# Kernel optimization log

Measured on AMD Instinct MI355X. Metric: run time of the kernel, lower is better.

## Reference

```python
import jax, jax.numpy as jnp
import numpy as np
from jax import lax

B, C, D, H, W = 2, 1, 128, 128, 128
CONSCIOUSNESS_WEIGHT = 0.1


def _field(depth, height, width, dtype):
    # sin(2*pi*(d+h+w)/(D+H+W)) broadcast over batch/channel
    d = jnp.arange(depth, dtype=dtype)[:, None, None]
    h = jnp.arange(height, dtype=dtype)[None, :, None]
    w = jnp.arange(width, dtype=dtype)[None, None, :]
    phase = 2.0 * jnp.pi * (d + h + w) / (depth + height + width)
    return jnp.sin(phase)  # [D,H,W]


def _conv3d(x, w, b):
    y = lax.conv_general_dilated(
        x, w, window_strides=(1, 1, 1), padding='SAME',
        dimension_numbers=('NCDHW', 'OIDHW', 'NCDHW'))
    return y + b[None, :, None, None, None]


def setup_inputs() -> dict:
    key = jax.random.key(0)
    ks = jax.random.split(key, 4)
    fan1 = 1 * 27
    fan2 = 8 * 27
    fan3 = 16 * 27
    return {
        'cube_data': jax.random.normal(ks[0], (B, C, D, H, W), dtype=jnp.float32),
        'w1': jax.random.normal(ks[1], (8, 1, 3, 3, 3), dtype=jnp.float32) / np.sqrt(fan1),
        'b1': jnp.zeros((8,), dtype=jnp.float32),
        'w2': jax.random.normal(ks[2], (16, 8, 3, 3, 3), dtype=jnp.float32) / np.sqrt(fan2),
        'b2': jnp.zeros((16,), dtype=jnp.float32),
        'w3': jax.random.normal(ks[3], (1, 16, 3, 3, 3), dtype=jnp.float32) / np.sqrt(fan3),
        'b3': jnp.zeros((1,), dtype=jnp.float32),
    }


def reference(cube_data, w1, b1, w2, b2, w3, b3):
    _, _, d, h, w = cube_data.shape
    field = _field(d, h, w, cube_data.dtype)[None, None]  # [1,1,D,H,W]
    integrated = cube_data * (1.0 + CONSCIOUSNESS_WEIGHT * field)
    x = jax.nn.relu(_conv3d(integrated, w1, b1))
    x = jax.nn.relu(_conv3d(x, w2, b2))
    x = jnp.tanh(_conv3d(x, w3, b3))
    return x
```

## Files before the change

### kernel.cpp

```cpp
#include <hip/hip_runtime.h>
#include <hip/hip_fp16.h>

#define VOX (128 * 128 * 128)
#define P 130
#define PP (P * P)
#define PVOX (P * P * P)
#define LROW 130
#define PLANE (6 * LROW)

typedef unsigned short u16;
typedef _Float16 f16x2 __attribute__((ext_vector_type(2)));
typedef _Float16 f16x8 __attribute__((ext_vector_type(8)));
typedef __attribute__((ext_vector_type(4))) float f32x4;

__device__ __forceinline__ u16 f2h(float f) {
    return __builtin_bit_cast(unsigned short, (_Float16)f);
}
__device__ __forceinline__ unsigned pkh_relu(float a, float b) {
    float ra = a > 0.f ? a : 0.f, rb = b > 0.f ? b : 0.f;
    return (unsigned)f2h(ra) | ((unsigned)f2h(rb) << 16);
}
__device__ __forceinline__ f16x2 h2(unsigned u) { return __builtin_bit_cast(f16x2, u); }

__device__ __forceinline__ float dot2(unsigned a, unsigned b, float c) {
#if __has_builtin(__builtin_amdgcn_fdot2)
    return __builtin_amdgcn_fdot2(h2(a), h2(b), c, false);
#else
    f16x2 av = h2(a), bv = h2(b);
    c = fmaf((float)av.x, (float)bv.x, c);
    return fmaf((float)av.y, (float)bv.y, c);
#endif
}

__device__ __forceinline__ float fast_tanh(float x) {
    float e = __expf(2.0f * x);
    return 1.0f - 2.0f * __builtin_amdgcn_rcpf(1.0f + e);
}

__device__ __forceinline__ void gload_lds16(const u16* g, u16* l) {
    __builtin_amdgcn_global_load_lds(
        (const __attribute__((address_space(1))) unsigned int*)g,
        (__attribute__((address_space(3))) unsigned int*)l,
        16, 0, 0);
}

__global__ __launch_bounds__(256) void integrate_kernel(
    const float* __restrict__ in, u16* __restrict__ x0,
    const float* __restrict__ w1, const float* __restrict__ w2,
    const float* __restrict__ w3, u16* __restrict__ w2frag,
    unsigned* __restrict__ w3p, float* __restrict__ w1c,
    u16* __restrict__ x1, u16* __restrict__ x2) {
    int i = blockIdx.x * 256 + threadIdx.x;
    if (i < 3584) {
        int j = i & 7, l = (i >> 3) & 63, s = i >> 9;
        int tap = s * 4 + (l >> 4), oc = l & 15;
        float v = (tap < 27) ? w2[(oc * 8 + j) * 27 + tap] : 0.0f;
        w2frag[i] = f2h(v);
    }
    if (i < 216) {
        int tap = i >> 3, j = i & 7;
        w3p[i] = (unsigned)f2h(w3[(2 * j) * 27 + tap]) |
                 ((unsigned)f2h(w3[(2 * j + 1) * 27 + tap]) << 16);
        int c = i & 7;
        w1c[i] = w1[c * 27 + tap];
    }
    if (i >= PVOX) return;
    int d = i / PP;
    int r = i - d * PP;
    int h = r / P;
    int w = r - h * P;
    const bool interior = (d >= 1 && d <= 128 && h >= 1 && h <= 128 && w >= 1 && w <= 128);
    float v = 0.0f;
    if (interior) {
        int s = (d - 1) + (h - 1) + (w - 1);
        float fld = 1.0f + 0.1f * __sinf(6.283185307179586f * (float)s / 384.0f);
        v = in[(size_t)(d - 1) * 16384 + (h - 1) * 128 + (w - 1)] * fld;
    } else {
        uint4 z = {0u, 0u, 0u, 0u};
        *(uint4*)(x1 + (size_t)i * 8) = z;
        *(uint4*)(x2 + (size_t)i * 16) = z;
        *(uint4*)(x2 + (size_t)i * 16 + 8) = z;
    }
    x0[i] = f2h(v);
}

__global__ __launch_bounds__(256) void integrate_light_kernel(
    const float* __restrict__ in, u16* __restrict__ x0) {
    const int i = blockIdx.x * 256 + threadIdx.x;
    const int d = i >> 14, h = (i >> 7) & 127, w = i & 127;
    const int s = d + h + w;
    const float fld = 1.0f + 0.1f * __sinf((float)s * 0.016362461737446838f);
    x0[(size_t)(d + 1) * PP + (h + 1) * P + (w + 1)] = f2h(in[i] * fld);
}

__global__ __launch_bounds__(256) void conv1_kernel(
    const u16* __restrict__ x0, const float* __restrict__ w1c,
    const float* __restrict__ b1, u16* __restrict__ x1) {
    const int t = blockIdx.x * 256 + threadIdx.x;
    const int w0 = (t & 63) * 2;
    const int h0 = ((t >> 6) & 31) * 4;
    const int d = t >> 11;

    float acc[4][2][8];
#pragma unroll
    for (int c = 0; c < 8; ++c) {
        const float b = b1[c];
#pragma unroll
        for (int i = 0; i < 4; ++i) { acc[i][0][c] = b; acc[i][1][c] = b; }
    }

#pragma unroll
    for (int dz = 0; dz < 3; ++dz) {
        const u16* zb = x0 + (size_t)(d + dz) * PP + (size_t)h0 * P + w0;
        const float* wz = w1c + dz * 9 * 8;
#pragma unroll
        for (int r = 0; r < 6; ++r) {
            const u16* rp = zb + r * P;
            const unsigned u0 = *(const unsigned*)rp;
            const unsigned u1 = *(const unsigned*)(rp + 2);
            float vv[4];
            vv[0] = (float)h2(u0).x; vv[1] = (float)h2(u0).y;
            vv[2] = (float)h2(u1).x; vv[3] = (float)h2(u1).y;
#pragma unroll
            for (int dy = 0; dy < 3; ++dy) {
                const int i = r - dy;
                if (i < 0 || i > 3) continue;
#pragma unroll
                for (int dx = 0; dx < 3; ++dx) {
                    const float a0 = vv[dx];
                    const float a1 = vv[dx + 1];
                    const float* wp = wz + (dy * 3 + dx) * 8;
#pragma unroll
                    for (int c = 0; c < 8; ++c) {
                        const float wt = wp[c];
                        acc[i][0][c] = fmaf(wt, a0, acc[i][0][c]);
                        acc[i][1][c] = fmaf(wt, a1, acc[i][1][c]);
                    }
                }
            }
        }
    }
    const size_t e0 = ((size_t)(d + 1) * P + (h0 + 1)) * P + (w0 + 1);
#pragma unroll
    for (int i = 0; i < 4; ++i) {
        uint4 oA, oB;
        oA.x = pkh_relu(acc[i][0][0], acc[i][0][1]);
        oA.y = pkh_relu(acc[i][0][2], acc[i][0][3]);
        oA.z = pkh_relu(acc[i][0][4], acc[i][0][5]);
        oA.w = pkh_relu(acc[i][0][6], acc[i][0][7]);
        oB.x = pkh_relu(acc[i][1][0], acc[i][1][1]);
        oB.y = pkh_relu(acc[i][1][2], acc[i][1][3]);
        oB.z = pkh_relu(acc[i][1][4], acc[i][1][5]);
        oB.w = pkh_relu(acc[i][1][6], acc[i][1][7]);
        *(uint4*)(x1 + (e0 + (size_t)i * P) * 8) = oA;
        *(uint4*)(x1 + (e0 + (size_t)i * P + 1) * 8) = oB;
    }
}

__global__ __launch_bounds__(256) void conv2_mfma_kernel(
    const u16* __restrict__ x1, const u16* __restrict__ w2frag,
    const float* __restrict__ b2, u16* __restrict__ x2) {
    __shared__ u16 sm[4 * PLANE * 8];

    const int tid = threadIdx.x;
    const int lane = tid & 63;
    const int wv = tid >> 6;
    const int q = lane >> 4;
    const int mi = lane & 15;
    const int D0 = (blockIdx.x >> 5) * 8;
    const int h0 = (blockIdx.x & 31) * 4;

    f16x8 wf[7];
#pragma unroll
    for (int s = 0; s < 7; ++s)
        wf[s] = *(const f16x8*)(w2frag + (size_t)(s * 64 + lane) * 8);

#pragma unroll
    for (int p = 0; p < 3; ++p) {
        const int pd = D0 + p;
        const int slot = pd & 3;
        const u16* gb = x1 + ((size_t)(pd * P + h0) * P) * 8;
        u16* lb = sm + (size_t)slot * PLANE * 8;
#pragma unroll
        for (int k = 0; k < 3; ++k) {
            const int u0 = wv * 64 + k * 256;
            gload_lds16(gb + (size_t)(u0 + lane) * 8, lb + (size_t)u0 * 8);
        }
        if (wv == 0 && lane < PLANE - 768)
            gload_lds16(gb + (size_t)(768 + lane) * 8, lb + (size_t)768 * 8);
    }
    __syncthreads();

    const float4 bv = *(const float4*)(b2 + q * 4);

#pragma unroll 1
    for (int i = 0; i < 8; ++i) {
        const int dout = D0 + i;

        if (i < 7) {
            const int pd = dout + 3;
            const int slot = pd & 3;
            const u16* gb = x1 + ((size_t)(pd * P + h0) * P) * 8;
            u16* lb = sm + (size_t)slot * PLANE * 8;
#pragma unroll
            for (int k = 0; k < 3; ++k) {
                const int u0 = wv * 64 + k * 256;
                gload_lds16(gb + (size_t)(u0 + lane) * 8, lb + (size_t)u0 * 8);
            }
            if (wv == 0 && lane < PLANE - 768)
                gload_lds16(gb + (size_t)(768 + lane) * 8, lb + (size_t)768 * 8);
        }

        f32x4 acc[8];
#pragma unroll
        for (int t = 0; t < 8; ++t) acc[t] = (f32x4){0.f, 0.f, 0.f, 0.f};

#pragma unroll
        for (int s = 0; s < 7; ++s) {
            int tap = s * 4 + q;
            if (tap > 26) tap = 26;
            const int dz = tap / 9;
            const int rem = tap - dz * 9;
            const int dy = rem / 3;
            const int dx = rem - dy * 3;
            const int slot = (dout + dz) & 3;
            const u16* bp = sm + ((size_t)(slot * 6 + wv + dy) * LROW + (mi + dx)) * 8;
#pragma unroll
            for (int t = 0; t < 8; ++t) {
                f16x8 act = *(const f16x8*)(bp + t * 128);
                acc[t] = __builtin_amdgcn_mfma_f32_16x16x32_f16(wf[s], act, acc[t], 0, 0, 0);
            }
        }

        const size_t obase = ((size_t)(dout + 1) * P + (h0 + wv + 1)) * P + 1;
#pragma unroll
        for (int t = 0; t < 8; ++t) {
            uint2 o;
            o.x = pkh_relu(acc[t][0] + bv.x, acc[t][1] + bv.y);
            o.y = pkh_relu(acc[t][2] + bv.z, acc[t][3] + bv.w);
            *(uint2*)(x2 + (obase + 16 * t + mi) * 16 + q * 4) = o;
        }

        if (i < 7) __syncthreads();
    }
}

__global__ __launch_bounds__(256) void conv3_kernel(
    const u16* __restrict__ x2, const unsigned* __restrict__ w3p,
    const float* __restrict__ b3, float* __restrict__ out) {
    const int t = blockIdx.x * 256 + threadIdx.x;
    const int w = t & 127;
    const int h0 = ((t >> 7) & 31) * 4;
    const int d0 = (t >> 12) * 2;

    float accA[2][4], accB[2][4];
#pragma unroll
    for (int dd = 0; dd < 2; ++dd)
#pragma unroll
        for (int i = 0; i < 4; ++i) { accA[dd][i] = 0.f; accB[dd][i] = 0.f; }

#pragma unroll 1
    for (int z = 0; z < 4; ++z) {
        const u16* zb = x2 + ((size_t)((d0 + z) * P + h0) * P + w) * 16;
#pragma unroll
        for (int r = 0; r < 6; ++r) {
            const u16* rp = zb + (size_t)r * (P * 16);
            const uint4 c0l = *(const uint4*)(rp);
            const uint4 c0h = *(const uint4*)(rp + 8);
            const uint4 c1l = *(const uint4*)(rp + 16);
            const uint4 c1h = *(const uint4*)(rp + 24);
            const uint4 c2l = *(const uint4*)(rp + 32);
            const uint4 c2h = *(const uint4*)(rp + 40);
#pragma unroll
            for (int dd = 0; dd < 2; ++dd) {
                const int dz = z - dd;
                if (dz < 0 || dz > 2) continue;
                const unsigned* wz = w3p + dz * 9 * 8;
#pragma unroll
                for (int dy = 0; dy < 3; ++dy) {
                    const int i = r - dy;
                    if (i < 0 || i > 3) continue;
                    const unsigned* wp = wz + dy * 3 * 8;
                    float a = accA[dd][i], b = accB[dd][i];
                    a = dot2(c0l.x, wp[0], a);  b = dot2(c0l.y, wp[1], b);
                    a = dot2(c0l.z, wp[2], a);  b = dot2(c0l.w, wp[3], b);
                    a = dot2(c0h.x, wp[4], a);  b = dot2(c0h.y, wp[5], b);
                    a = dot2(c0h.z, wp[6], a);  b = dot2(c0h.w, wp[7], b);
                    a = dot2(c1l.x, wp[8], a);  b = dot2(c1l.y, wp[9], b);
                    a = dot2(c1l.z, wp[10], a); b = dot2(c1l.w, wp[11], b);
                    a = dot2(c1h.x, wp[12], a); b = dot2(c1h.y, wp[13], b);
                    a = dot2(c1h.z, wp[14], a); b = dot2(c1h.w, wp[15], b);
                    a = dot2(c2l.x, wp[16], a); b = dot2(c2l.y, wp[17], b);
                    a = dot2(c2l.z, wp[18], a); b = dot2(c2l.w, wp[19], b);
                    a = dot2(c2h.x, wp[20], a); b = dot2(c2h.y, wp[21], b);
                    a = dot2(c2h.z, wp[22], a); b = dot2(c2h.w, wp[23], b);
                    accA[dd][i] = a; accB[dd][i] = b;
                }
            }
        }
    }
    const float bias = b3[0];
#pragma unroll
    for (int dd = 0; dd < 2; ++dd) {
        const size_t obase = (size_t)((d0 + dd) * 128 + h0) * 128 + w;
#pragma unroll
        for (int i = 0; i < 4; ++i)
            out[obase + (size_t)i * 128] = fast_tanh(accA[dd][i] + accB[dd][i] + bias);
    }
}

extern "C" void kernel_launch(void* const* d_in, const int* in_sizes, int n_in,
                              void* d_out, int out_size, void* d_ws, size_t ws_size,
                              hipStream_t stream) {
    const float* cube = (const float*)d_in[0];
    const float* w1 = (const float*)d_in[1];
    const float* b1 = (const float*)d_in[2];
    const float* w2 = (const float*)d_in[3];
    const float* b2 = (const float*)d_in[4];
    const float* w3 = (const float*)d_in[5];
    const float* b3 = (const float*)d_in[6];
    float* out = (float*)d_out;

    char* ws = (char*)d_ws;
    u16* w2frag = (u16*)ws;
    unsigned* w3p = (unsigned*)(ws + 7168);
    float* w1c = (float*)(ws + 8032);
    u16* x0 = (u16*)(ws + 16384);
    u16* x1 = (u16*)(ws + 16384 + (size_t)PVOX * sizeof(u16));
    u16* x2 = (u16*)(ws + 16384 + (size_t)PVOX * sizeof(u16) + (size_t)PVOX * 8 * sizeof(u16));

    for (int b = 0; b < 2; ++b) {
        if (b == 0) {
            integrate_kernel<<<dim3((PVOX + 255) / 256), dim3(256), 0, stream>>>(
                cube, x0, w1, w2, w3, w2frag, w3p, w1c, x1, x2);
        } else {
            integrate_light_kernel<<<dim3(VOX / 256), dim3(256), 0, stream>>>(
                cube + (size_t)VOX, x0);
        }
        conv1_kernel<<<dim3(VOX / 8 / 256), dim3(256), 0, stream>>>(x0, w1c, b1, x1);
        conv2_mfma_kernel<<<dim3(512), dim3(256), 0, stream>>>(x1, w2frag, b2, x2);
        conv3_kernel<<<dim3(VOX / 8 / 256), dim3(256), 0, stream>>>(
            x2, w3p, b3, out + (size_t)b * VOX);
    }
}
```

Before: 216.1 us.

## Use fine-grained vmcnt waits in conv2, merge batch-1 integrate into conv3

In conv2, the full __syncthreads after the prefetch is replaced by explicit s_waitcnt vmcnt counts plus raw s_barrier. Each iteration now waits only for the plane it needs while the next plane's async LDS loads stay in flight. Conv3 drops from 4 to 2 output rows per thread, doubling the grid for more parallelism at the cost of more redundant row loads. The batch-1 integrate kernel is folded into conv3's batch-0 launch as extra blocks, removing one launch. The hand-counted vmcnt values are fragile and could break correctness if the compiler reorders or adds loads.

After: 220.9 us. 1.02x slower.

```diff
diff --git a/kernel.cpp b/kernel.cpp
--- a/kernel.cpp
+++ b/kernel.cpp
@@ -43,6 +43,8 @@
         (__attribute__((address_space(3))) unsigned int*)l,
         16, 0, 0);
 }
+
+#define WAITCNT(N) asm volatile("s_waitcnt vmcnt(" #N ")" ::: "memory")
 
 __global__ __launch_bounds__(256) void integrate_kernel(
     const float* __restrict__ in, u16* __restrict__ x0,
@@ -84,15 +86,6 @@
     x0[i] = f2h(v);
 }
 
-__global__ __launch_bounds__(256) void integrate_light_kernel(
-    const float* __restrict__ in, u16* __restrict__ x0) {
-    const int i = blockIdx.x * 256 + threadIdx.x;
-    const int d = i >> 14, h = (i >> 7) & 127, w = i & 127;
-    const int s = d + h + w;
-    const float fld = 1.0f + 0.1f * __sinf((float)s * 0.016362461737446838f);
-    x0[(size_t)(d + 1) * PP + (h + 1) * P + (w + 1)] = f2h(in[i] * fld);
-}
-
 __global__ __launch_bounds__(256) void conv1_kernel(
     const u16* __restrict__ x0, const float* __restrict__ w1c,
     const float* __restrict__ b1, u16* __restrict__ x1) {
@@ -189,7 +182,8 @@
         if (wv == 0 && lane < PLANE - 768)
             gload_lds16(gb + (size_t)(768 + lane) * 8, lb + (size_t)768 * 8);
     }
-    __syncthreads();
+    WAITCNT(0);
+    __builtin_amdgcn_s_barrier();
 
     const float4 bv = *(const float4*)(b2 + q * 4);
 
@@ -210,6 +204,11 @@
             if (wv == 0 && lane < PLANE - 768)
                 gload_lds16(gb + (size_t)(768 + lane) * 8, lb + (size_t)768 * 8);
         }
+
+        if (i == 0)     WAITCNT(3);
+        else if (i < 7) WAITCNT(19);
+        else            WAITCNT(16);
+        __builtin_amdgcn_s_barrier();
 
         f32x4 acc[8];
 #pragma unroll
@@ -241,29 +240,39 @@
             *(uint2*)(x2 + (obase + 16 * t + mi) * 16 + q * 4) = o;
         }
 
-        if (i < 7) __syncthreads();
+        if (i < 7) __builtin_amdgcn_s_barrier();
     }
 }
 
 __global__ __launch_bounds__(256) void conv3_kernel(
     const u16* __restrict__ x2, const unsigned* __restrict__ w3p,
-    const float* __restrict__ b3, float* __restrict__ out) {
-    const int t = blockIdx.x * 256 + threadIdx.x;
+    const float* __restrict__ b3, float* __restrict__ out,
+    const float* __restrict__ in_b1, u16* __restrict__ x0) {
+    const int bid = blockIdx.x;
+    if (bid >= 2048) {
+        const int i = (bid - 2048) * 256 + threadIdx.x;
+        const int d = i >> 14, h = (i >> 7) & 127, w = i & 127;
+        const float fld =
+            1.0f + 0.1f * __sinf((float)(d + h + w) * 0.016362461737446838f);
+        x0[(size_t)(d + 1) * PP + (h + 1) * P + (w + 1)] = f2h(in_b1[i] * fld);
+        return;
+    }
+    const int t = bid * 256 + threadIdx.x;
     const int w = t & 127;
-    const int h0 = ((t >> 7) & 31) * 4;
-    const int d0 = (t >> 12) * 2;
-
-    float accA[2][4], accB[2][4];
+    const int h0 = ((t >> 7) & 63) * 2;
+    const int d0 = (t >> 13) * 2;
+
+    float accA[2][2], accB[2][2];
 #pragma unroll
     for (int dd = 0; dd < 2; ++dd)
 #pragma unroll
-        for (int i = 0; i < 4; ++i) { accA[dd][i] = 0.f; accB[dd][i] = 0.f; }
+        for (int i = 0; i < 2; ++i) { accA[dd][i] = 0.f; accB[dd][i] = 0.f; }
 
 #pragma unroll 1
     for (int z = 0; z < 4; ++z) {
         const u16* zb = x2 + ((size_t)((d0 + z) * P + h0) * P + w) * 16;
 #pragma unroll
-        for (int r = 0; r < 6; ++r) {
+        for (int r = 0; r < 4; ++r) {
             const u16* rp = zb + (size_t)r * (P * 16);
             const uint4 c0l = *(const uint4*)(rp);
             const uint4 c0h = *(const uint4*)(rp + 8);
@@ -279,7 +288,7 @@
 #pragma unroll
                 for (int dy = 0; dy < 3; ++dy) {
                     const int i = r - dy;
-                    if (i < 0 || i > 3) continue;
+                    if (i < 0 || i > 1) continue;
                     const unsigned* wp = wz + dy * 3 * 8;
                     float a = accA[dd][i], b = accB[dd][i];
                     a = dot2(c0l.x, wp[0], a);  b = dot2(c0l.y, wp[1], b);
@@ -304,7 +313,7 @@
     for (int dd = 0; dd < 2; ++dd) {
         const size_t obase = (size_t)((d0 + dd) * 128 + h0) * 128 + w;
 #pragma unroll
-        for (int i = 0; i < 4; ++i)
+        for (int i = 0; i < 2; ++i)
             out[obase + (size_t)i * 128] = fast_tanh(accA[dd][i] + accB[dd][i] + bias);
     }
 }
@@ -333,13 +342,15 @@
         if (b == 0) {
             integrate_kernel<<<dim3((PVOX + 255) / 256), dim3(256), 0, stream>>>(
                 cube, x0, w1, w2, w3, w2frag, w3p, w1c, x1, x2);
-        } else {
-            integrate_light_kernel<<<dim3(VOX / 256), dim3(256), 0, stream>>>(
-                cube + (size_t)VOX, x0);
         }
         conv1_kernel<<<dim3(VOX / 8 / 256), dim3(256), 0, stream>>>(x0, w1c, b1, x1);
         conv2_mfma_kernel<<<dim3(512), dim3(256), 0, stream>>>(x1, w2frag, b2, x2);
-        conv3_kernel<<<dim3(VOX / 8 / 256), dim3(256), 0, stream>>>(
-            x2, w3p, b3, out + (size_t)b * VOX);
-    }
-}
+        if (b == 0) {
+            conv3_kernel<<<dim3(2048 + VOX / 256), dim3(256), 0, stream>>>(
+                x2, w3p, b3, out, cube + (size_t)VOX, x0);
+        } else {
+            conv3_kernel<<<dim3(2048), dim3(256), 0, stream>>>(
+                x2, w3p, b3, out + (size_t)VOX, cube + (size_t)VOX, x0);
+        }
+    }
+}
```
